# Kernel optimization log

Hardware: AMD Instinct MI355X
Metric: run time of the kernel (lower is better)

## Reference

```python
import jax, jax.numpy as jnp
import numpy as np

B = 64        # number of graphs
NPG = 2048    # nodes per graph (equal-size; math identical to padded ragged original)
N = B * NPG
C = 64        # in_channels == out_channels
H = 4         # num_heads
D = 64        # out_channels per head


def setup_inputs() -> dict:
    key = jax.random.key(0)
    k1, k2, k3, k4, k5 = jax.random.split(key, 5)
    s = 1.0 / np.sqrt(C)
    return {
        "x": jax.random.normal(k1, (N, C), dtype=jnp.float32),
        "Wq_w": jax.random.uniform(k2, (H * D, C), jnp.float32, -s, s),
        "Wq_b": jax.random.uniform(k3, (H * D,), jnp.float32, -s, s),
        "Wk_w": jax.random.uniform(k4, (H * D, C), jnp.float32, -s, s),
        "Wk_b": jax.random.uniform(k5, (H * D,), jnp.float32, -s, s),
        "n_nodes": jnp.full((B,), NPG, dtype=jnp.int32),
    }


def reference(x, Wq_w, Wq_b, Wk_w, Wk_b, n_nodes):
    # Linear projections (torch Linear: x @ W^T + b), reshape to [N, H, D]
    q = (x @ Wq_w.T + Wq_b).reshape(N, H, D)
    k = (x @ Wk_w.T + Wk_b).reshape(N, H, D)
    v = jnp.broadcast_to(x[:, None, :], (N, H, C))  # value = x repeated per head

    # L2-normalize q, k along feature dim
    q = q / jnp.linalg.norm(q, axis=2, keepdims=True)
    k = k / jnp.linalg.norm(k, axis=2, keepdims=True)

    # segment views: [B, n, H, D]
    qb = q.reshape(B, NPG, H, D)
    kb = k.reshape(B, NPG, H, D)
    vb = v.reshape(B, NPG, H, C)

    # per-graph k^T v outer product: [B, H, D, C]
    kv = jnp.einsum('bnhd,bnhe->bhde', kb, vb)
    k_sum = kb.sum(axis=1)  # [B, H, D]
    v_sum = vb.sum(axis=1)  # [B, H, C]

    numerator = jnp.einsum('bnhd,bhde->bnhe', qb, kv) + v_sum[:, None]  # [B, n, H, C]
    nn = n_nodes.astype(x.dtype)
    denominator = jnp.einsum('bnhd,bhd->bnh', qb, k_sum) + nn[:, None, None]  # [B, n, H]

    out = numerator / denominator[..., None]
    return out.reshape(N, H * C)
```

## Files before the change

kernel.cpp:

```cpp
#include <hip/hip_runtime.h>

#define BB    64
#define NPG   2048
#define TILE  128
#define NTILES (NPG / TILE)
#define XP    72
#define TP    136
#define QP    104

typedef short bf16x8 __attribute__((ext_vector_type(8)));
typedef float f32x4  __attribute__((ext_vector_type(4)));
typedef unsigned short u16x8 __attribute__((ext_vector_type(8)));
typedef unsigned short u16x4 __attribute__((ext_vector_type(4)));

__device__ __forceinline__ unsigned short f2b(float f) {
    unsigned int u = __float_as_uint(f);
    return (unsigned short)((u + 0x7FFFu + ((u >> 16) & 1u)) >> 16);
}

extern "C" __global__ __launch_bounds__(512, 2)
void kv_kernel(const float* __restrict__ x,
               const float* __restrict__ Wk_w,
               const float* __restrict__ Wk_b,
               float* __restrict__ kvt)
{
    __shared__ __align__(16) unsigned short xlds[TILE * XP];
    __shared__ __align__(16) unsigned short xt[80 * TP];
    __shared__ __align__(16) unsigned short kt[80 * TP];

    const int t  = threadIdx.x;
    const int l  = t & 63;
    const int w  = t >> 6;
    const int lr = l & 15;
    const int lg = l >> 4;
    const int bh = blockIdx.x;
    const int b  = bh >> 2;
    const int h  = bh & 3;

    bf16x8 wf[4][2];
    float  bias[4][4];
#pragma unroll
    for (int mt = 0; mt < 4; ++mt) {
        const float* wp = Wk_w + (size_t)(h * 64 + mt * 16 + lr) * 64;
#pragma unroll
        for (int ks = 0; ks < 2; ++ks) {
            const float* p = wp + ks * 32 + lg * 8;
            bf16x8 f;
#pragma unroll
            for (int j = 0; j < 8; ++j) f[j] = (short)f2b(p[j]);
            wf[mt][ks] = f;
        }
#pragma unroll
        for (int i = 0; i < 4; ++i) bias[mt][i] = Wk_b[h * 64 + mt * 16 + 4 * lg + i];
    }

    for (int idx = t; idx < 16 * TP; idx += 512) {
        int rr = idx / TP;
        int cc = idx - rr * TP;
        unsigned short v = (rr == 0 && cc < TILE) ? (unsigned short)0x3F80u : (unsigned short)0u;
        xt[(64 + rr) * TP + cc] = v;
        kt[(64 + rr) * TP + cc] = v;
    }

    int cts[4], dts[4];
#pragma unroll
    for (int ti = 0; ti < 3; ++ti) {
        int tau = w + 8 * ti;
        int q5  = tau / 5;
        cts[ti] = q5;
        dts[ti] = tau - 5 * q5;
    }
    cts[3] = 4; dts[3] = 4;

    f32x4 kvacc[4] = {};

    const int cp = t & 63;
    const int n0 = (t >> 6) * 16;

    const float4* xg0 = (const float4*)(x + (size_t)b * NPG * 64);

    for (int tt = 0; tt < NTILES; ++tt) {
        __syncthreads();

        const float4* xg = xg0 + (size_t)tt * TILE * 16;
#pragma unroll
        for (int j = 0; j < 4; ++j) {
            float4 v = xg[j * 512 + t];
            int n = j * 32 + (t >> 4);
            int c = (t & 15) * 4;
            u16x4 pv = { f2b(v.x), f2b(v.y), f2b(v.z), f2b(v.w) };
            *(u16x4*)&xlds[n * XP + c] = pv;
        }
        __syncthreads();

        {
            u16x8 w0, w1;
#pragma unroll
            for (int k2 = 0; k2 < 8; ++k2) w0[k2] = xlds[(n0 + k2) * XP + cp];
#pragma unroll
            for (int k2 = 0; k2 < 8; ++k2) w1[k2] = xlds[(n0 + 8 + k2) * XP + cp];
            *(u16x8*)&xt[cp * TP + n0]     = w0;
            *(u16x8*)&xt[cp * TP + n0 + 8] = w1;
        }

        f32x4 pacc[4] = {};
        const int ncol = w * 16 + lr;
#pragma unroll
        for (int ks = 0; ks < 2; ++ks) {
            bf16x8 xb = *(const bf16x8*)&xlds[ncol * XP + ks * 32 + lg * 8];
#pragma unroll
            for (int mt = 0; mt < 4; ++mt)
                pacc[mt] = __builtin_amdgcn_mfma_f32_16x16x32_bf16(wf[mt][ks], xb, pacc[mt], 0, 0, 0);
        }
        float ss = 0.f;
#pragma unroll
        for (int mt = 0; mt < 4; ++mt)
#pragma unroll
            for (int i = 0; i < 4; ++i) {
                float v = pacc[mt][i] + bias[mt][i];
                pacc[mt][i] = v;
                ss = fmaf(v, v, ss);
            }
        ss += __shfl_xor(ss, 16, 64);
        ss += __shfl_xor(ss, 32, 64);
        float sc = rsqrtf(ss);
#pragma unroll
        for (int mt = 0; mt < 4; ++mt)
#pragma unroll
            for (int i = 0; i < 4; ++i)
                kt[(mt * 16 + 4 * lg + i) * TP + ncol] = f2b(pacc[mt][i] * sc);
        __syncthreads();

#pragma unroll
        for (int ks = 0; ks < 4; ++ks) {
            const int ko = ks * 32 + lg * 8;
            bf16x8 a0 = *(const bf16x8*)&xt[(cts[0] * 16 + lr) * TP + ko];
            bf16x8 b0 = *(const bf16x8*)&kt[(dts[0] * 16 + lr) * TP + ko];
            kvacc[0] = __builtin_amdgcn_mfma_f32_16x16x32_bf16(a0, b0, kvacc[0], 0, 0, 0);
            bf16x8 a1 = *(const bf16x8*)&xt[(cts[1] * 16 + lr) * TP + ko];
            bf16x8 b1 = *(const bf16x8*)&kt[(dts[1] * 16 + lr) * TP + ko];
            kvacc[1] = __builtin_amdgcn_mfma_f32_16x16x32_bf16(a1, b1, kvacc[1], 0, 0, 0);
            bf16x8 a2 = *(const bf16x8*)&xt[(cts[2] * 16 + lr) * TP + ko];
            bf16x8 b2 = *(const bf16x8*)&kt[(dts[2] * 16 + lr) * TP + ko];
            kvacc[2] = __builtin_amdgcn_mfma_f32_16x16x32_bf16(a2, b2, kvacc[2], 0, 0, 0);
            if (w == 0) {
                bf16x8 a3 = *(const bf16x8*)&xt[(64 + lr) * TP + ko];
                bf16x8 b3 = *(const bf16x8*)&kt[(64 + lr) * TP + ko];
                kvacc[3] = __builtin_amdgcn_mfma_f32_16x16x32_bf16(a3, b3, kvacc[3], 0, 0, 0);
            }
        }
    }

#pragma unroll
    for (int ti = 0; ti < 3; ++ti) {
        float* dst = kvt + ((size_t)bh * 80 + cts[ti] * 16 + 4 * lg) * 80 + dts[ti] * 16 + lr;
#pragma unroll
        for (int i = 0; i < 4; ++i) dst[i * 80] = kvacc[ti][i];
    }
    if (w == 0) {
        float* dst = kvt + ((size_t)bh * 80 + 64 + 4 * lg) * 80 + 64 + lr;
#pragma unroll
        for (int i = 0; i < 4; ++i) dst[i * 80] = kvacc[3][i];
    }
}

extern "C" __global__ __launch_bounds__(512, 2)
void out_kernel(const float* __restrict__ x,
                const float* __restrict__ Wq_w,
                const float* __restrict__ Wq_b,
                const float* __restrict__ kvt,
                float* __restrict__ out)
{
    __shared__ __align__(16) unsigned short xlds[TILE * XP];
    __shared__ __align__(16) unsigned short qlds[TILE * QP];

    const int t  = threadIdx.x;
    const int l  = t & 63;
    const int w  = t >> 6;
    const int lr = l & 15;
    const int lg = l >> 4;
    const int bh = blockIdx.x;
    const int b  = bh >> 2;
    const int h  = bh & 3;

    bf16x8 wf[4][2];
    float  bias[4][4];
#pragma unroll
    for (int mt = 0; mt < 4; ++mt) {
        const float* wp = Wq_w + (size_t)(h * 64 + mt * 16 + lr) * 64;
#pragma unroll
        for (int ks = 0; ks < 2; ++ks) {
            const float* p = wp + ks * 32 + lg * 8;
            bf16x8 f;
#pragma unroll
            for (int j = 0; j < 8; ++j) f[j] = (short)f2b(p[j]);
            wf[mt][ks] = f;
        }
#pragma unroll
        for (int i = 0; i < 4; ++i) bias[mt][i] = Wq_b[h * 64 + mt * 16 + 4 * lg + i];
    }

    bf16x8 kvf[5][3];
#pragma unroll
    for (int ct = 0; ct < 5; ++ct) {
        const float* kp = kvt + ((size_t)bh * 80 + ct * 16 + lr) * 80;
#pragma unroll
        for (int ks = 0; ks < 2; ++ks) {
            const float* p = kp + ks * 32 + lg * 8;
            bf16x8 f;
#pragma unroll
            for (int j = 0; j < 8; ++j) f[j] = (short)f2b(p[j]);
            kvf[ct][ks] = f;
        }
        bf16x8 f2 = {0, 0, 0, 0, 0, 0, 0, 0};
        if (lg == 0) f2[0] = (short)f2b(kp[64]);
        kvf[ct][2] = f2;
    }

    for (int idx = t; idx < TILE * 32; idx += 512) {
        int n  = idx >> 5;
        int cc = 64 + (idx & 31);
        qlds[n * QP + cc] = (cc == 64) ? (unsigned short)0x3F80u : (unsigned short)0u;
    }

    const float4* xg0 = (const float4*)(x + (size_t)b * NPG * 64);

    for (int tt = 0; tt < NTILES; ++tt) {
        __syncthreads();

        const float4* xg = xg0 + (size_t)tt * TILE * 16;
#pragma unroll
        for (int j = 0; j < 4; ++j) {
            float4 v = xg[j * 512 + t];
            int n = j * 32 + (t >> 4);
            int c = (t & 15) * 4;
            u16x4 pv = { f2b(v.x), f2b(v.y), f2b(v.z), f2b(v.w) };
            *(u16x4*)&xlds[n * XP + c] = pv;
        }
        __syncthreads();

        f32x4 pacc[4] = {};
        const int ncol = w * 16 + lr;
#pragma unroll
        for (int ks = 0; ks < 2; ++ks) {
            bf16x8 xb = *(const bf16x8*)&xlds[ncol * XP + ks * 32 + lg * 8];
#pragma unroll
            for (int mt = 0; mt < 4; ++mt)
                pacc[mt] = __builtin_amdgcn_mfma_f32_16x16x32_bf16(wf[mt][ks], xb, pacc[mt], 0, 0, 0);
        }
        float ss = 0.f;
#pragma unroll
        for (int mt = 0; mt < 4; ++mt)
#pragma unroll
            for (int i = 0; i < 4; ++i) {
                float v = pacc[mt][i] + bias[mt][i];
                pacc[mt][i] = v;
                ss = fmaf(v, v, ss);
            }
        ss += __shfl_xor(ss, 16, 64);
        ss += __shfl_xor(ss, 32, 64);
        float sc = rsqrtf(ss);
#pragma unroll
        for (int mt = 0; mt < 4; ++mt)
#pragma unroll
            for (int i = 0; i < 4; ++i)
                qlds[ncol * QP + mt * 16 + 4 * lg + i] = f2b(pacc[mt][i] * sc);
        __syncthreads();

        f32x4 nacc[5] = {};
#pragma unroll
        for (int ks = 0; ks < 3; ++ks) {
            bf16x8 qa = *(const bf16x8*)&qlds[(w * 16 + lr) * QP + ks * 32 + lg * 8];
#pragma unroll
            for (int ct = 0; ct < 5; ++ct)
                nacc[ct] = __builtin_amdgcn_mfma_f32_16x16x32_bf16(qa, kvf[ct][ks], nacc[ct], 0, 0, 0);
        }

        const int nrow = tt * TILE + w * 16;
        float* op = out + ((size_t)b * NPG + nrow) * 256 + h * 64;
#pragma unroll
        for (int i = 0; i < 4; ++i) {
            float den  = __shfl(nacc[4][i], (l & 48), 64);
            float rden = 1.0f / den;
#pragma unroll
            for (int ct = 0; ct < 4; ++ct)
                op[(size_t)(4 * lg + i) * 256 + ct * 16 + lr] = nacc[ct][i] * rden;
        }
    }
}

extern "C" void kernel_launch(void* const* d_in, const int* in_sizes, int n_in,
                              void* d_out, int out_size, void* d_ws, size_t ws_size,
                              hipStream_t stream) {
    const float* x    = (const float*)d_in[0];
    const float* Wq_w = (const float*)d_in[1];
    const float* Wq_b = (const float*)d_in[2];
    const float* Wk_w = (const float*)d_in[3];
    const float* Wk_b = (const float*)d_in[4];
    float* out = (float*)d_out;
    float* kvt = (float*)d_ws;

    hipLaunchKernelGGL(kv_kernel,  dim3(256), dim3(512), 0, stream, x, Wk_w, Wk_b, kvt);
    hipLaunchKernelGGL(out_kernel, dim3(256), dim3(512), 0, stream, x, Wq_w, Wq_b, kvt, out);
}
```

Baseline: 255.8 us.

## Split each graph into node chunks, prefetch x tiles, and map blocks XCD-aware

Both kernels now split each graph's 2048 nodes into two chunks, so the grid doubles to 512 blocks. kv_kernel writes a partial kv matrix per chunk, and out_kernel sums the two partials when it loads them. Each loop iteration prefetches the next x tile into registers while the current tile is being computed, which removes one barrier per iteration. Block indices are decoded so that blocks of the same graph share an XCD, and launch bounds are raised to 4 blocks per CU to allow more occupancy. The cost is a doubled kv workspace and an extra partial-sum read in out_kernel.

New measurement: 354.5 us. +38.6%, slower.

```diff
diff --git a/kernel.cpp b/kernel.cpp
--- a/kernel.cpp
+++ b/kernel.cpp
@@ -1,12 +1,13 @@
 #include <hip/hip_runtime.h>
 
-#define BB    64
-#define NPG   2048
-#define TILE  128
-#define NTILES (NPG / TILE)
-#define XP    72
-#define TP    136
-#define QP    104
+#define BB     64
+#define NPG    2048
+#define TILE   128
+#define CHUNKS 2
+#define TPB    8
+#define XP     72
+#define TP     136
+#define QP     104
 
 typedef short bf16x8 __attribute__((ext_vector_type(8)));
 typedef float f32x4  __attribute__((ext_vector_type(4)));
@@ -18,7 +19,27 @@
     return (unsigned short)((u + 0x7FFFu + ((u >> 16) & 1u)) >> 16);
 }
 
-extern "C" __global__ __launch_bounds__(512, 2)
+__device__ __forceinline__ void stage_write(unsigned short* xlds, const float4* rx, int t) {
+#pragma unroll
+    for (int j = 0; j < 4; ++j) {
+        int n = j * 32 + (t >> 4);
+        int c = (t & 15) * 4;
+        u16x4 pv = { f2b(rx[j].x), f2b(rx[j].y), f2b(rx[j].z), f2b(rx[j].w) };
+        *(u16x4*)&xlds[n * XP + c] = pv;
+    }
+}
+
+__device__ __forceinline__ void decode_bid(int g, int& b, int& h, int& chunk, int& bh) {
+    int xcd  = g & 7;
+    int rest = g >> 3;
+    int bhi  = rest & 7;
+    h     = (rest >> 3) & 3;
+    chunk = rest >> 5;
+    b     = bhi * 8 + xcd;
+    bh    = b * 4 + h;
+}
+
+extern "C" __global__ __launch_bounds__(512, 4)
 void kv_kernel(const float* __restrict__ x,
                const float* __restrict__ Wk_w,
                const float* __restrict__ Wk_b,
@@ -33,9 +54,8 @@
     const int w  = t >> 6;
     const int lr = l & 15;
     const int lg = l >> 4;
-    const int bh = blockIdx.x;
-    const int b  = bh >> 2;
-    const int h  = bh & 3;
+    int b, h, chunk, bh;
+    decode_bid(blockIdx.x, b, h, chunk, bh);
 
     bf16x8 wf[4][2];
     float  bias[4][4];
@@ -77,21 +97,19 @@
     const int cp = t & 63;
     const int n0 = (t >> 6) * 16;
 
-    const float4* xg0 = (const float4*)(x + (size_t)b * NPG * 64);
-
-    for (int tt = 0; tt < NTILES; ++tt) {
-        __syncthreads();
-
-        const float4* xg = xg0 + (size_t)tt * TILE * 16;
-#pragma unroll
-        for (int j = 0; j < 4; ++j) {
-            float4 v = xg[j * 512 + t];
-            int n = j * 32 + (t >> 4);
-            int c = (t & 15) * 4;
-            u16x4 pv = { f2b(v.x), f2b(v.y), f2b(v.z), f2b(v.w) };
-            *(u16x4*)&xlds[n * XP + c] = pv;
-        }
-        __syncthreads();
+    const float4* xg0 = (const float4*)(x + ((size_t)b * NPG + (size_t)chunk * (NPG / CHUNKS)) * 64);
+
+    float4 rx[4];
+#pragma unroll
+    for (int j = 0; j < 4; ++j) rx[j] = xg0[j * 512 + t];
+    stage_write(xlds, rx, t);
+    __syncthreads();
+
+    for (int tt = 0; tt < TPB; ++tt) {
+        const int ttn = (tt + 1 < TPB) ? tt + 1 : tt;
+        const float4* xg = xg0 + (size_t)ttn * TILE * 16;
+#pragma unroll
+        for (int j = 0; j < 4; ++j) rx[j] = xg[j * 512 + t];
 
         {
             u16x8 w0, w1;
@@ -149,22 +167,26 @@
                 kvacc[3] = __builtin_amdgcn_mfma_f32_16x16x32_bf16(a3, b3, kvacc[3], 0, 0, 0);
             }
         }
-    }
-
+
+        stage_write(xlds, rx, t);
+        __syncthreads();
+    }
+
+    float* base = kvt + (size_t)(chunk * 256 + bh) * 80 * 80;
 #pragma unroll
     for (int ti = 0; ti < 3; ++ti) {
-        float* dst = kvt + ((size_t)bh * 80 + cts[ti] * 16 + 4 * lg) * 80 + dts[ti] * 16 + lr;
+        float* dst = base + (size_t)(cts[ti] * 16 + 4 * lg) * 80 + dts[ti] * 16 + lr;
 #pragma unroll
         for (int i = 0; i < 4; ++i) dst[i * 80] = kvacc[ti][i];
     }
     if (w == 0) {
-        float* dst = kvt + ((size_t)bh * 80 + 64 + 4 * lg) * 80 + 64 + lr;
+        float* dst = base + (size_t)(64 + 4 * lg) * 80 + 64 + lr;
 #pragma unroll
         for (int i = 0; i < 4; ++i) dst[i * 80] = kvacc[3][i];
     }
 }
 
-extern "C" __global__ __launch_bounds__(512, 2)
+extern "C" __global__ __launch_bounds__(512, 4)
 void out_kernel(const float* __restrict__ x,
                 const float* __restrict__ Wq_w,
                 const float* __restrict__ Wq_b,
@@ -179,9 +201,8 @@
     const int w  = t >> 6;
     const int lr = l & 15;
     const int lg = l >> 4;
-    const int bh = blockIdx.x;
-    const int b  = bh >> 2;
-    const int h  = bh & 3;
+    int b, h, chunk, bh;
+    decode_bid(blockIdx.x, b, h, chunk, bh);
 
     bf16x8 wf[4][2];
     float  bias[4][4];
@@ -203,17 +224,19 @@
     bf16x8 kvf[5][3];
 #pragma unroll
     for (int ct = 0; ct < 5; ++ct) {
-        const float* kp = kvt + ((size_t)bh * 80 + ct * 16 + lr) * 80;
-#pragma unroll
-        for (int ks = 0; ks < 2; ++ks) {
-            const float* p = kp + ks * 32 + lg * 8;
+        const float* kp0 = kvt + (size_t)bh * 6400 + (size_t)(ct * 16 + lr) * 80;
+        const float* kp1 = kp0 + (size_t)256 * 6400;
+#pragma unroll
+        for (int ks = 0; ks < 2; ++ks) {
+            const float* p0 = kp0 + ks * 32 + lg * 8;
+            const float* p1 = kp1 + ks * 32 + lg * 8;
             bf16x8 f;
 #pragma unroll
-            for (int j = 0; j < 8; ++j) f[j] = (short)f2b(p[j]);
+            for (int j = 0; j < 8; ++j) f[j] = (short)f2b(p0[j] + p1[j]);
             kvf[ct][ks] = f;
         }
         bf16x8 f2 = {0, 0, 0, 0, 0, 0, 0, 0};
-        if (lg == 0) f2[0] = (short)f2b(kp[64]);
+        if (lg == 0) f2[0] = (short)f2b(kp0[64] + kp1[64]);
         kvf[ct][2] = f2;
     }
 
@@ -223,21 +246,19 @@
         qlds[n * QP + cc] = (cc == 64) ? (unsigned short)0x3F80u : (unsigned short)0u;
     }
 
-    const float4* xg0 = (const float4*)(x + (size_t)b * NPG * 64);
-
-    for (int tt = 0; tt < NTILES; ++tt) {
-        __syncthreads();
-
-        const float4* xg = xg0 + (size_t)tt * TILE * 16;
-#pragma unroll
-        for (int j = 0; j < 4; ++j) {
-            float4 v = xg[j * 512 + t];
-            int n = j * 32 + (t >> 4);
-            int c = (t & 15) * 4;
-            u16x4 pv = { f2b(v.x), f2b(v.y), f2b(v.z), f2b(v.w) };
-            *(u16x4*)&xlds[n * XP + c] = pv;
-        }
-        __syncthreads();
+    const float4* xg0 = (const float4*)(x + ((size_t)b * NPG + (size_t)chunk * (NPG / CHUNKS)) * 64);
+
+    float4 rx[4];
+#pragma unroll
+    for (int j = 0; j < 4; ++j) rx[j] = xg0[j * 512 + t];
+    stage_write(xlds, rx, t);
+    __syncthreads();
+
+    for (int tt = 0; tt < TPB; ++tt) {
+        const int ttn = (tt + 1 < TPB) ? tt + 1 : tt;
+        const float4* xg = xg0 + (size_t)ttn * TILE * 16;
+#pragma unroll
+        for (int j = 0; j < 4; ++j) rx[j] = xg[j * 512 + t];
 
         f32x4 pacc[4] = {};
         const int ncol = w * 16 + lr;
@@ -276,7 +297,7 @@
                 nacc[ct] = __builtin_amdgcn_mfma_f32_16x16x32_bf16(qa, kvf[ct][ks], nacc[ct], 0, 0, 0);
         }
 
-        const int nrow = tt * TILE + w * 16;
+        const size_t nrow = (size_t)chunk * (NPG / CHUNKS) + (size_t)tt * TILE + w * 16;
         float* op = out + ((size_t)b * NPG + nrow) * 256 + h * 64;
 #pragma unroll
         for (int i = 0; i < 4; ++i) {
@@ -286,6 +307,9 @@
             for (int ct = 0; ct < 4; ++ct)
                 op[(size_t)(4 * lg + i) * 256 + ct * 16 + lr] = nacc[ct][i] * rden;
         }
+
+        stage_write(xlds, rx, t);
+        __syncthreads();
     }
 }
 
@@ -300,6 +324,6 @@
     float* out = (float*)d_out;
     float* kvt = (float*)d_ws;
 
-    hipLaunchKernelGGL(kv_kernel,  dim3(256), dim3(512), 0, stream, x, Wk_w, Wk_b, kvt);
-    hipLaunchKernelGGL(out_kernel, dim3(256), dim3(512), 0, stream, x, Wq_w, Wq_b, kvt, out);
-}
+    hipLaunchKernelGGL(kv_kernel,  dim3(512), dim3(512), 0, stream, x, Wk_w, Wk_b, kvt);
+    hipLaunchKernelGGL(out_kernel, dim3(512), dim3(512), 0, stream, x, Wq_w, Wq_b, kvt, out);
+}
```
